# Optimization experiments

Measured on AMD Instinct MI355X. Metric: run time of the kernel, lower is better.

The kernel has to match this reference:

```python
import jax, jax.numpy as jnp
import numpy as np
from jax import lax

WHISPER_DIM, WAVLM_DIM, MUQ_DIM = 1280, 1024, 1024
CODEBOOK_SIZE, CODEBOOK_DIM = 8192, 256
B, T_W, T_M = 8, 2048, 1024  # T_w = T_wl = 2048 @50Hz, muq @25Hz -> T_m = 1024
CONCAT_DIM = WHISPER_DIM + WAVLM_DIM + MUQ_DIM


def setup_inputs() -> dict:
    key = jax.random.key(0)
    ks = jax.random.split(key, 10)
    s = 0.02
    return {
        "whisper_feat": jax.random.normal(ks[0], (B, T_W, WHISPER_DIM), jnp.float32),
        "wavlm_feat": jax.random.normal(ks[1], (B, T_W, WAVLM_DIM), jnp.float32),
        "muq_feat": jax.random.normal(ks[2], (B, T_M, MUQ_DIM), jnp.float32),
        # Conv1d weights, torch layout (out_ch, in_ch, k)
        "w_conv_w": jax.random.normal(ks[3], (WHISPER_DIM, WHISPER_DIM, 4), jnp.float32) * s,
        "w_conv_b": jnp.zeros((WHISPER_DIM,), jnp.float32),
        "wl_conv_w": jax.random.normal(ks[4], (WAVLM_DIM, WAVLM_DIM, 4), jnp.float32) * s,
        "wl_conv_b": jnp.zeros((WAVLM_DIM,), jnp.float32),
        # Linear: torch layout (out_features, in_features)
        "proj_w": jax.random.normal(ks[5], (CODEBOOK_DIM, CONCAT_DIM), jnp.float32) * s,
        "proj_b": jnp.zeros((CODEBOOK_DIM,), jnp.float32),
        "codebook": jax.random.normal(ks[6], (CODEBOOK_SIZE, CODEBOOK_DIM), jnp.float32) * 0.02,
    }


def _conv1d_s2(x_btc, w_oik, b):
    # x: (B, T, C) -> (B, C, T) conv k=4 s=2 p=1 -> (B, T//2, C)
    y = lax.conv_general_dilated(
        x_btc.transpose(0, 2, 1), w_oik,
        window_strides=(2,), padding=[(1, 1)],
        dimension_numbers=("NCH", "OIH", "NCH"))
    return (y + b[None, :, None]).transpose(0, 2, 1)


def reference(whisper_feat, wavlm_feat, muq_feat, w_conv_w, w_conv_b,
              wl_conv_w, wl_conv_b, proj_w, proj_b, codebook):
    w = _conv1d_s2(whisper_feat, w_conv_w, w_conv_b)   # (B, 1024, 1280)
    wl = _conv1d_s2(wavlm_feat, wl_conv_w, wl_conv_b)  # (B, 1024, 1024)
    m = muq_feat                                        # (B, 1024, 1024)
    min_len = min(w.shape[1], wl.shape[1], m.shape[1])
    concat = jnp.concatenate([w[:, :min_len], wl[:, :min_len], m[:, :min_len]], axis=-1)
    z_e = jnp.einsum("btc,dc->btd", concat, proj_w) + proj_b  # (B, T, D)

    # VQ: squared-Euclidean argmin against the codebook (same argmin as cdist)
    Bsz, T, D = z_e.shape
    z_flat = z_e.reshape(-1, D)
    d2 = (jnp.sum(z_flat * z_flat, axis=-1, keepdims=True)
          - 2.0 * z_flat @ codebook.T
          + jnp.sum(codebook * codebook, axis=-1)[None, :])  # (B*T, K)
    codes = jnp.argmin(d2, axis=-1)                     # (B*T,)
    z_q = codebook[codes].reshape(Bsz, T, D)
    z_q_st = z_e + lax.stop_gradient(z_q - z_e)
    commit_loss = jnp.mean(jnp.square(z_e - lax.stop_gradient(z_q)))
    return z_q_st, codes.reshape(Bsz, T), commit_loss
```

## Files before the change

kernel.cpp:

```cpp
#include <hip/hip_runtime.h>
#include <cstdint>
#include <cstddef>

typedef unsigned short u16;
typedef __attribute__((ext_vector_type(8))) short bf16x8;
typedef __attribute__((ext_vector_type(4))) float f32x4;
typedef unsigned int u32;
typedef __attribute__((address_space(1))) const u32 gu32;
typedef __attribute__((address_space(3))) u32 lu32;

__device__ __forceinline__ void gload_lds16(const void* g, void* l) {
    __builtin_amdgcn_global_load_lds((gu32*)g, (lu32*)l, 16, 0, 0);
}

__device__ __forceinline__ u16 f2bf(float v) {
    u32 u = __float_as_uint(v);
    return (u16)((u + 0x7fffu + ((u >> 16) & 1u)) >> 16);
}
__device__ __forceinline__ float bf2f(u16 h) { return __uint_as_float(((u32)h) << 16); }

__device__ __forceinline__ void split3(float f, u16& h1, u16& h2, u16& h3) {
    h1 = f2bf(f); float r = f - bf2f(h1);
    h2 = f2bf(r); r -= bf2f(h2);
    h3 = f2bf(r);
}

__device__ __forceinline__ void mfma6(f32x4& c, bf16x8 a1, bf16x8 a2, bf16x8 a3,
                                      bf16x8 b1, bf16x8 b2, bf16x8 b3) {
    c = __builtin_amdgcn_mfma_f32_16x16x32_bf16(a1, b1, c, 0, 0, 0);
    c = __builtin_amdgcn_mfma_f32_16x16x32_bf16(a1, b2, c, 0, 0, 0);
    c = __builtin_amdgcn_mfma_f32_16x16x32_bf16(a2, b1, c, 0, 0, 0);
    c = __builtin_amdgcn_mfma_f32_16x16x32_bf16(a1, b3, c, 0, 0, 0);
    c = __builtin_amdgcn_mfma_f32_16x16x32_bf16(a3, b1, c, 0, 0, 0);
    c = __builtin_amdgcn_mfma_f32_16x16x32_bf16(a2, b2, c, 0, 0, 0);
}

__global__ __launch_bounds__(256)
void split_x8t(const float* __restrict__ x, u16* __restrict__ p0,
               size_t pstr, int I) {
    __shared__ u16 tl[12288];
    const int b = blockIdx.x / 33, blk = blockIdx.x - b * 33;
    const int o0 = blk * 64;
    const int nval = (o0 + 64 <= 2050) ? 64 : (2050 - o0);
    const int c0 = blockIdx.y << 6;
    const int tid = threadIdx.x;
    const int r = tid >> 2, c4 = tid & 3;

    if (r < nval) {
        int local = o0 + r;
        int parity = local >= 1025 ? 1 : 0;
        int idx = local - parity * 1025;
        int prow = 2 * idx + parity;
        bool pad = (prow == 0) || (prow == 2049);
        int s = pad ? 0 : (prow - 1);
        const float* src = x + (size_t)(b * 2048 + s) * I + c0;
#pragma unroll
        for (int k = 0; k < 4; k++) {
            int cf4 = c4 + k * 4;
            float4 v = make_float4(0.f, 0.f, 0.f, 0.f);
            if (!pad) v = *reinterpret_cast<const float4*>(src + cf4 * 4);
            float vals[4] = {v.x, v.y, v.z, v.w};
            int base = ((cf4 >> 1) * 64 + r) * 8 + (cf4 & 1) * 4;
#pragma unroll
            for (int q = 0; q < 4; q++) {
                u16 h1, h2, h3; split3(vals[q], h1, h2, h3);
                tl[base + q]        = h1;
                tl[4096 + base + q] = h2;
                tl[8192 + base + q] = h3;
            }
        }
    }
    __syncthreads();
#pragma unroll
    for (int e = tid; e < 1536; e += 256) {
        int p = e >> 9, rem = e & 511;
        int gs = rem >> 6, rr = rem & 63;
        if (rr < nval) {
            size_t dst = (size_t)p * pstr +
                         (size_t)((c0 >> 3) + gs) * 131200 +
                         (size_t)(b * 2050 + o0 + rr) * 8;
            *reinterpret_cast<bf16x8*>(&p0[dst]) =
                *reinterpret_cast<const bf16x8*>(&tl[p * 4096 + (gs * 64 + rr) * 8]);
        }
    }
}

__global__ __launch_bounds__(256)
void split_rows8t(const float* __restrict__ in, u16* __restrict__ p0,
                  size_t pstr, int R, int C) {
    __shared__ u16 tl[12288];
    const int r0 = blockIdx.x << 6;
    const int c0 = blockIdx.y << 6;
    const int tid = threadIdx.x;
    const int r = tid >> 2, c4 = tid & 3;
    const float* src = in + (size_t)(r0 + r) * C + c0;
#pragma unroll
    for (int k = 0; k < 4; k++) {
        int cf4 = c4 + k * 4;
        float4 v = *reinterpret_cast<const float4*>(src + cf4 * 4);
        float vals[4] = {v.x, v.y, v.z, v.w};
        int base = ((cf4 >> 1) * 64 + r) * 8 + (cf4 & 1) * 4;
#pragma unroll
        for (int q = 0; q < 4; q++) {
            u16 h1, h2, h3; split3(vals[q], h1, h2, h3);
            tl[base + q]        = h1;
            tl[4096 + base + q] = h2;
            tl[8192 + base + q] = h3;
        }
    }
    __syncthreads();
#pragma unroll
    for (int e = tid; e < 1536; e += 256) {
        int p = e >> 9, rem = e & 511;
        int gs = rem >> 6, rr = rem & 63;
        size_t dst = (size_t)p * pstr +
                     ((size_t)((c0 >> 3) + gs) * R + (r0 + rr)) * 8;
        *reinterpret_cast<bf16x8*>(&p0[dst]) =
            *reinterpret_cast<const bf16x8*>(&tl[p * 4096 + (gs * 64 + rr) * 8]);
    }
}

__global__ __launch_bounds__(256)
void split_weightT8t(const float* __restrict__ w, u16* __restrict__ p0,
                     size_t pstr, int I, int O) {
    __shared__ u16 tl[12288];
    const int o0 = blockIdx.x << 6;
    const int c0 = blockIdx.y << 6;
    const int G = I >> 3;
    const int tid = threadIdx.x;
    const int r = tid >> 2, c4 = tid & 3;
    for (int kcv = 0; kcv < 4; kcv++) {
#pragma unroll
        for (int k = 0; k < 4; k++) {
            int cf4 = c4 + k * 4;
#pragma unroll
            for (int q = 0; q < 4; q++) {
                int i = c0 + cf4 * 4 + q;
                float f = w[((size_t)(o0 + r) * I + i) * 4 + kcv];
                u16 h1, h2, h3; split3(f, h1, h2, h3);
                int base = ((cf4 >> 1) * 64 + r) * 8 + (cf4 & 1) * 4 + q;
                tl[base]        = h1;
                tl[4096 + base] = h2;
                tl[8192 + base] = h3;
            }
        }
        __syncthreads();
        for (int e = tid; e < 1536; e += 256) {
            int p = e >> 9, rem = e & 511;
            int gs = rem >> 6, rr = rem & 63;
            size_t dst = (size_t)p * pstr +
                         ((size_t)(kcv * G + (c0 >> 3) + gs) * O + (o0 + rr)) * 8;
            *reinterpret_cast<bf16x8*>(&p0[dst]) =
                *reinterpret_cast<const bf16x8*>(&tl[p * 4096 + (gs * 64 + rr) * 8]);
        }
        __syncthreads();
    }
}

__global__ void cnorm_kernel(const float* __restrict__ cb, float* __restrict__ cn) {
    int w = threadIdx.x >> 6, lane = threadIdx.x & 63;
    int row = blockIdx.x * 4 + w;
    float4 v = *reinterpret_cast<const float4*>(&cb[(size_t)row * 256 + lane * 4]);
    float s = v.x * v.x + v.y * v.y + v.z * v.z + v.w * v.w;
#pragma unroll
    for (int off = 32; off; off >>= 1) s += __shfl_xor(s, off);
    if (lane == 0) cn[row] = s;
}

__global__ __launch_bounds__(256, 2)
void conv_mfma6(const u16* __restrict__ xs, unsigned pstr_x,
                const u16* __restrict__ wt, unsigned pstr_w,
                const float* __restrict__ bias,
                u16* __restrict__ outp, unsigned pstr_o,
                int I, int O) {
    __shared__ u16 lds[32768];
    const int m0 = blockIdx.x << 7;
    const int n0 = blockIdx.y << 7;
    const int tid = threadIdx.x, lane = tid & 63, wv = tid >> 6;
    const int wr = ((wv >> 1) & 1) << 6, wc = (wv & 1) << 6;
    const int fr = lane & 15, fkg = lane >> 4;
    const int b = m0 >> 10, t0 = m0 & 1023;
    const int G = I >> 3;
    const int SL = 131200;
    const int NIT = G;
    const int npt = G >> 2;

    const u16* srcp[8];
    int dsto[8];
    int inc;
#pragma unroll
    for (int j = 0; j < 8; j++) {
        int kg = j >> 1, half = j & 1;
        int r = half * 64 + lane;
        if (wv < 2) {
            srcp[j] = xs + (size_t)wv * pstr_x + (size_t)kg * SL +
                      (size_t)(b * 2050 + t0 + r) * 8;
        } else {
            srcp[j] = wt + (size_t)(wv - 2) * pstr_w + (size_t)kg * (O * 8) +
                      (size_t)(n0 + r) * 8;
        }
        dsto[j] = wv * 4096 + j * 512;
    }
    inc = (wv < 2) ? 4 * SL : O * 32;

    const u16* pa3 = xs + 2 * (size_t)pstr_x + (size_t)fkg * SL +
                     (size_t)(b * 2050 + t0 + wr + fr) * 8;
    const u16* pb3 = wt + 2 * (size_t)pstr_w + (size_t)fkg * (O * 8) +
                     (size_t)(n0 + wc + fr) * 8;

    f32x4 acc[4][4];
#pragma unroll
    for (int i = 0; i < 4; i++)
#pragma unroll
        for (int j = 0; j < 4; j++) acc[i][j] = (f32x4){0.f, 0.f, 0.f, 0.f};

#pragma unroll
    for (int j = 0; j < 8; j++) {
        gload_lds16(srcp[j], &lds[dsto[j]]);
        srcp[j] += inc;
    }
    __syncthreads();

    int scnt = npt - 1, skcv = 0;
    int dcnt = npt, dkcv = 0;
    int cur = 0;

    for (int it = 0; it < NIT; ++it) {
        const u16* lb = &lds[cur * 16384];
        bf16x8 a1[4], a2[4], b1[4], b2[4];
#pragma unroll
        for (int fm = 0; fm < 4; fm++) {
            int aidx = fkg * 1024 + (wr + fm * 16 + fr) * 8;
            a1[fm] = *reinterpret_cast<const bf16x8*>(lb + aidx);
            a2[fm] = *reinterpret_cast<const bf16x8*>(lb + 4096 + aidx);
        }
#pragma unroll
        for (int fn = 0; fn < 4; fn++) {
            int bidx = fkg * 1024 + (wc + fn * 16 + fr) * 8;
            b1[fn] = *reinterpret_cast<const bf16x8*>(lb + 8192 + bidx);
            b2[fn] = *reinterpret_cast<const bf16x8*>(lb + 12288 + bidx);
        }
        if (it + 1 < NIT) {
#pragma unroll
            for (int j = 0; j < 8; j++) {
                gload_lds16(srcp[j], &lds[(cur ^ 1) * 16384 + dsto[j]]);
                srcp[j] += inc;
            }
            if (wv < 2) {
                if (--scnt == 0) {
                    int d = ((skcv == 1) ? -8192 : 8200) - (int)pstr_x;
#pragma unroll
                    for (int j = 0; j < 8; j++) srcp[j] += d;
                    skcv++; scnt = npt;
                }
            }
        }
        bf16x8 da3[4], db3[4];
#pragma unroll
        for (int fm = 0; fm < 4; fm++)
            da3[fm] = *reinterpret_cast<const bf16x8*>(pa3 + fm * 128);
#pragma unroll
        for (int fn = 0; fn < 4; fn++)
            db3[fn] = *reinterpret_cast<const bf16x8*>(pb3 + fn * 128);
        pa3 += 4 * SL;
        pb3 += O * 32;
        if (--dcnt == 0) {
            pa3 += ((dkcv == 1) ? -8192 : 8200) - (int)pstr_x;
            dkcv++; dcnt = npt;
        }
#pragma unroll
        for (int fm = 0; fm < 4; fm++)
#pragma unroll
            for (int fn = 0; fn < 4; fn++)
                mfma6(acc[fm][fn], a1[fm], a2[fm], da3[fm],
                      b1[fn], b2[fn], db3[fn]);
        __syncthreads();
        cur ^= 1;
    }

    u16 (*eld)[32][132] = (u16 (*)[32][132])lds;
    float bv[4];
#pragma unroll
    for (int fn = 0; fn < 4; fn++) bv[fn] = bias[n0 + wc + fn * 16 + fr];
    const int srb = (wr >> 6) * 16 + fkg * 4;
#pragma unroll
    for (int fm = 0; fm < 4; fm++) {
#pragma unroll
        for (int fn = 0; fn < 4; fn++) {
            int cl = wc + fn * 16 + fr;
#pragma unroll
            for (int j = 0; j < 4; j++) {
                float f = acc[fm][fn][j] + bv[fn];
                u16 h1, h2, h3; split3(f, h1, h2, h3);
                eld[0][srb + j][cl] = h1;
                eld[1][srb + j][cl] = h2;
                eld[2][srb + j][cl] = h3;
            }
        }
        __syncthreads();
#pragma unroll
        for (int q = 0; q < 6; q++) {
            int e = q * 256 + tid;
            int g = e / 96, rem = e - g * 96;
            int p = rem >> 5, sr = rem & 31;
            bf16x8 vv = *reinterpret_cast<const bf16x8*>(&eld[p][sr][g * 8]);
            int rowg = m0 + ((sr >> 4) << 6) + fm * 16 + (sr & 15);
            size_t addr = (size_t)p * pstr_o +
                          (size_t)((n0 >> 3) + g) * 65536 + (size_t)rowg * 8;
            *reinterpret_cast<bf16x8*>(&outp[addr]) = vv;
        }
        __syncthreads();
    }
}

__global__ __launch_bounds__(256, 3)
void proj_mfma5(const u16* __restrict__ sA, const u16* __restrict__ sB,
                const u16* __restrict__ sM, const u16* __restrict__ wp,
                const float* __restrict__ bias, float* __restrict__ z_e,
                u16* __restrict__ zpl) {
    __shared__ u16 lds[24576];
    const int m0 = blockIdx.x << 7;
    const int n0 = blockIdx.y << 7;
    const int tid = threadIdx.x, lane = tid & 63, wv = tid >> 6;
    const int wr = ((wv >> 1) & 1) << 6, wc = (wv & 1) << 6;
    const int fr = lane & 15, fkg = lane >> 4;

    const u16* srcp[12];
    int dsto[12];
#pragma unroll
    for (int j = 0; j < 12; j++) {
        int ii = wv * 12 + j;
        int tile = ii >> 3, sub = ii & 7;
        int kg = sub >> 1, half = sub & 1;
        int r = half * 64 + lane;
        if (tile >= 3)
            srcp[j] = wp + (size_t)(tile - 3) * 851968 + (size_t)kg * 2048 +
                      (size_t)(n0 + r) * 8;
        else
            srcp[j] = nullptr;
        dsto[j] = tile * 4096 + sub * 512;
    }

    f32x4 acc[4][4];
#pragma unroll
    for (int i = 0; i < 4; i++)
#pragma unroll
        for (int j = 0; j < 4; j++) acc[i][j] = (f32x4){0.f, 0.f, 0.f, 0.f};

    const u16* segp[3] = {sA, sB, sM};
    const int segG[3] = {160, 128, 128};
    const unsigned segP[3] = {10485760u, 8388608u, 8388608u};

    for (int seg = 0; seg < 3; seg++) {
        const u16* sp = segp[seg];
        const unsigned sps = segP[seg];
#pragma unroll
        for (int j = 0; j < 12; j++) {
            int ii = wv * 12 + j;
            int tile = ii >> 3, sub = ii & 7;
            int kg = sub >> 1, half = sub & 1;
            int r = half * 64 + lane;
            if (tile < 3)
                srcp[j] = sp + (size_t)tile * sps + (size_t)kg * 65536 +
                          (size_t)(m0 + r) * 8;
        }
        const int niter = segG[seg] >> 2;
        for (int it = 0; it < niter; it++) {
#pragma unroll
            for (int j = 0; j < 12; j++) {
                gload_lds16(srcp[j], &lds[dsto[j]]);
                int ii = wv * 12 + j;
                srcp[j] += (ii >> 3) < 3 ? 262144 : 8192;
            }
            __syncthreads();
            bf16x8 bfr[3][4];
#pragma unroll
            for (int p = 0; p < 3; p++)
#pragma unroll
                for (int fn = 0; fn < 4; fn++)
                    bfr[p][fn] = *reinterpret_cast<const bf16x8*>(
                        &lds[(3 + p) * 4096 + fkg * 1024 + (wc + fn * 16 + fr) * 8]);
#pragma unroll
            for (int fm = 0; fm < 4; fm++) {
                int aidx = fkg * 1024 + (wr + fm * 16 + fr) * 8;
                bf16x8 a1 = *reinterpret_cast<const bf16x8*>(&lds[aidx]);
                bf16x8 a2 = *reinterpret_cast<const bf16x8*>(&lds[4096 + aidx]);
                bf16x8 a3 = *reinterpret_cast<const bf16x8*>(&lds[8192 + aidx]);
#pragma unroll
                for (int fn = 0; fn < 4; fn++)
                    mfma6(acc[fm][fn], a1, a2, a3, bfr[0][fn], bfr[1][fn], bfr[2][fn]);
            }
            __syncthreads();
        }
    }
    u16 (*eld)[32][132] = (u16 (*)[32][132])lds;
    float bv[4];
#pragma unroll
    for (int fn = 0; fn < 4; fn++) bv[fn] = bias[n0 + wc + fn * 16 + fr];
    const int srb = (wr >> 6) * 16 + fkg * 4;
#pragma unroll
    for (int fm = 0; fm < 4; fm++) {
#pragma unroll
        for (int fn = 0; fn < 4; fn++) {
            int cl = wc + fn * 16 + fr;
            int col = n0 + cl;
#pragma unroll
            for (int j = 0; j < 4; j++) {
                float f = acc[fm][fn][j] + bv[fn];
                int rowg = m0 + wr + fm * 16 + fkg * 4 + j;
                z_e[(size_t)rowg * 256 + col] = f;
                u16 h1, h2, h3; split3(f, h1, h2, h3);
                eld[0][srb + j][cl] = h1;
                eld[1][srb + j][cl] = h2;
                eld[2][srb + j][cl] = h3;
            }
        }
        __syncthreads();
#pragma unroll
        for (int q = 0; q < 6; q++) {
            int e = q * 256 + tid;
            int g = e / 96, rem = e - g * 96;
            int p = rem >> 5, sr = rem & 31;
            bf16x8 vv = *reinterpret_cast<const bf16x8*>(&eld[p][sr][g * 8]);
            int rowg = m0 + ((sr >> 4) << 6) + fm * 16 + (sr & 15);
            size_t addr = (size_t)p * 2097152 +
                          (size_t)((n0 >> 3) + g) * 65536 + (size_t)rowg * 8;
            *reinterpret_cast<bf16x8*>(&zpl[addr]) = vv;
        }
        __syncthreads();
    }
}

__global__ __launch_bounds__(256, 3)
void vq_mfma4(const u16* __restrict__ zpl, const u16* __restrict__ cbpl,
              const float* __restrict__ cn, double* __restrict__ pmin,
              int* __restrict__ pidx) {
    __shared__ __align__(16) char smem[49152];
    u16* lds = (u16*)smem;
    const int m0 = blockIdx.x << 7;
    const int n0 = blockIdx.y << 7;
    const int tid = threadIdx.x, lane = tid & 63, wv = tid >> 6;
    const int wr = ((wv >> 1) & 1) << 6, wc = (wv & 1) << 6;
    const int fr = lane & 15, fkg = lane >> 4;

    const u16* srcp[12];
    int dsto[12];
#pragma unroll
    for (int j = 0; j < 12; j++) {
        int ii = wv * 12 + j;
        int tile = ii >> 3, sub = ii & 7;
        int kg = sub >> 1, half = sub & 1;
        int r = half * 64 + lane;
        if (tile < 3)
            srcp[j] = zpl + (size_t)tile * 2097152 + (size_t)kg * 65536 +
                      (size_t)(m0 + r) * 8;
        else
            srcp[j] = cbpl + (size_t)(tile - 3) * 2097152 + (size_t)kg * 65536 +
                      (size_t)(n0 + r) * 8;
        dsto[j] = tile * 4096 + sub * 512;
    }

    f32x4 acc[4][4];
#pragma unroll
    for (int i = 0; i < 4; i++)
#pragma unroll
        for (int j = 0; j < 4; j++) acc[i][j] = (f32x4){0.f, 0.f, 0.f, 0.f};

    for (int kt = 0; kt < 256; kt += 32) {
#pragma unroll
        for (int j = 0; j < 12; j++) {
            gload_lds16(srcp[j], &lds[dsto[j]]);
            srcp[j] += 262144;
        }
        __syncthreads();
        bf16x8 bfr[3][4];
#pragma unroll
        for (int p = 0; p < 3; p++)
#pragma unroll
            for (int fn = 0; fn < 4; fn++)
                bfr[p][fn] = *reinterpret_cast<const bf16x8*>(
                    &lds[(3 + p) * 4096 + fkg * 1024 + (wc + fn * 16 + fr) * 8]);
#pragma unroll
        for (int fm = 0; fm < 4; fm++) {
            int aidx = fkg * 1024 + (wr + fm * 16 + fr) * 8;
            bf16x8 a1 = *reinterpret_cast<const bf16x8*>(&lds[aidx]);
            bf16x8 a2 = *reinterpret_cast<const bf16x8*>(&lds[4096 + aidx]);
            bf16x8 a3 = *reinterpret_cast<const bf16x8*>(&lds[8192 + aidx]);
#pragma unroll
            for (int fn = 0; fn < 4; fn++)
                mfma6(acc[fm][fn], a1, a2, a3, bfr[0][fn], bfr[1][fn], bfr[2][fn]);
        }
        __syncthreads();
    }
    double (*red_d)[32] = (double (*)[32])smem;
    int (*red_n)[32] = (int (*)[32])(smem + 32768);
#pragma unroll
    for (int fm = 0; fm < 4; fm++)
#pragma unroll
        for (int j = 0; j < 4; j++) {
            double best = 1e300; int bestn = 0x7fffffff;
#pragma unroll
            for (int fn = 0; fn < 4; fn++) {
                int gn = n0 + wc + fn * 16 + fr;
                double d = (double)cn[gn] - 2.0 * (double)acc[fm][fn][j];
                if (d < best || (d == best && gn < bestn)) { best = d; bestn = gn; }
            }
            int row = wr + fm * 16 + fkg * 4 + j;
            int cand = ((wv & 1) << 4) + fr;
            red_d[row][cand] = best; red_n[row][cand] = bestn;
        }
    __syncthreads();
    if (tid < 128) {
        double best = red_d[tid][0]; int bestn = red_n[tid][0];
#pragma unroll 4
        for (int k = 1; k < 32; k++) {
            double d = red_d[tid][k]; int n2 = red_n[tid][k];
            if (d < best || (d == best && n2 < bestn)) { best = d; bestn = n2; }
        }
        size_t idx = (size_t)(m0 + tid) * 64 + (n0 >> 7);
        pmin[idx] = best; pidx[idx] = bestn;
    }
}

__global__ void vq_finalize(const double* __restrict__ pmin, const int* __restrict__ pidx,
                            const float* __restrict__ z, const float* __restrict__ cb,
                            float* __restrict__ out, double* __restrict__ cpart) {
    int w = threadIdx.x >> 6, lane = threadIdx.x & 63;
    int m = blockIdx.x * 4 + w;
    double d = pmin[(size_t)m * 64 + lane];
    int n = pidx[(size_t)m * 64 + lane];
#pragma unroll
    for (int off = 32; off; off >>= 1) {
        double d2 = __shfl_xor(d, off);
        int n2 = __shfl_xor(n, off);
        if (d2 < d || (d2 == d && n2 < n)) { d = d2; n = n2; }
    }
    float4 cv = *reinterpret_cast<const float4*>(&cb[(size_t)n * 256 + lane * 4]);
    float4 zv = *reinterpret_cast<const float4*>(&z[(size_t)m * 256 + lane * 4]);
    *reinterpret_cast<float4*>(&out[(size_t)m * 256 + lane * 4]) = cv;
    float dx = zv.x - cv.x, dy = zv.y - cv.y, dz = zv.z - cv.z, dw = zv.w - cv.w;
    double s = (double)(dx * dx) + (double)(dy * dy) + (double)(dz * dz) + (double)(dw * dw);
#pragma unroll
    for (int off = 32; off; off >>= 1) s += __shfl_xor(s, off);
    if (lane == 0) {
        out[2097152 + m] = (float)n;
        cpart[m] = s;
    }
}

__global__ void vq_reduce(const double* __restrict__ cpart, float* __restrict__ out) {
    __shared__ double sm[256];
    double s = 0.0;
    for (int i = threadIdx.x; i < 8192; i += 256) s += cpart[i];
    sm[threadIdx.x] = s;
    __syncthreads();
    for (int off = 128; off; off >>= 1) {
        if ((int)threadIdx.x < off) sm[threadIdx.x] += sm[threadIdx.x + off];
        __syncthreads();
    }
    if (threadIdx.x == 0) out[2105344] = (float)(sm[0] / 2097152.0);
}

extern "C" void kernel_launch(void* const* d_in, const int* in_sizes, int n_in,
                              void* d_out, int out_size, void* d_ws, size_t ws_size,
                              hipStream_t stream) {
    (void)in_sizes; (void)n_in; (void)out_size; (void)ws_size;
    const float* whisper   = (const float*)d_in[0];
    const float* wavlm     = (const float*)d_in[1];
    const float* muq       = (const float*)d_in[2];
    const float* w_conv_w  = (const float*)d_in[3];
    const float* w_conv_b  = (const float*)d_in[4];
    const float* wl_conv_w = (const float*)d_in[5];
    const float* wl_conv_b = (const float*)d_in[6];
    const float* proj_w    = (const float*)d_in[7];
    const float* proj_b    = (const float*)d_in[8];
    const float* codebook  = (const float*)d_in[9];
    float* out = (float*)d_out;
    char* wsb = (char*)d_ws;

    u16*   xsA   = (u16*)(wsb + 0);
    u16*   wtbA  = (u16*)(wsb + 125952000);
    u16*   cApl  = (u16*)(wsb + 176259072);
    u16*   xsB   = (u16*)(wsb + 0);
    u16*   wtbB  = (u16*)(wsb + 100761600);
    u16*   cBpl  = (u16*)(wsb + 125927424);
    u16*   muqpl = (u16*)(wsb + 0);
    u16*   wtpPl = (u16*)(wsb + 50331648);
    float* z_e   = (float*)(wsb + 55443456);
    u16*   zpl   = (u16*)(wsb + 63832064);
    u16*   cbpl  = (u16*)(wsb + 76414976);
    float* cnorm = (float*)(wsb + 88997888);
    double* pmin = (double*)(wsb + 89030656);
    int*    pidx = (int*)(wsb + 93224960);
    double* cpart= (double*)(wsb + 95322112);

    split_x8t<<<dim3(264, 20), 256, 0, stream>>>(whisper, xsA, 20992000, 1280);
    split_weightT8t<<<dim3(20, 20), 256, 0, stream>>>(w_conv_w, wtbA, 6553600, 1280, 1280);
    conv_mfma6<<<dim3(64, 10), 256, 0, stream>>>(xsA, 20992000, wtbA, 6553600,
                                                 w_conv_b, cApl, 10485760, 1280, 1280);
    split_x8t<<<dim3(264, 16), 256, 0, stream>>>(wavlm, xsB, 16793600, 1024);
    split_weightT8t<<<dim3(16, 16), 256, 0, stream>>>(wl_conv_w, wtbB, 4194304, 1024, 1024);
    conv_mfma6<<<dim3(64, 8), 256, 0, stream>>>(xsB, 16793600, wtbB, 4194304,
                                                wl_conv_b, cBpl, 8388608, 1024, 1024);
    split_rows8t<<<dim3(128, 16), 256, 0, stream>>>(muq, muqpl, 8388608, 8192, 1024);
    split_rows8t<<<dim3(4, 52), 256, 0, stream>>>(proj_w, wtpPl, 851968, 256, 3328);
    proj_mfma5<<<dim3(64, 2), 256, 0, stream>>>(cApl, cBpl, muqpl, wtpPl, proj_b, z_e, zpl);
    split_rows8t<<<dim3(128, 4), 256, 0, stream>>>(codebook, cbpl, 2097152, 8192, 256);
    cnorm_kernel<<<2048, 256, 0, stream>>>(codebook, cnorm);
    vq_mfma4<<<dim3(64, 64), 256, 0, stream>>>(zpl, cbpl, cnorm, pmin, pidx);
    vq_finalize<<<2048, 256, 0, stream>>>(pmin, pidx, z_e, codebook, out, cpart);
    vq_reduce<<<1, 256, 0, stream>>>(cpart, out);
}
```

Baseline: 1.372 ms.

## Template conv GEMM on N-tile width and pack weights into contiguous per-tile slabs

The conv GEMM kernel now takes its N-tile width as a template parameter. The whisper conv uses 160-wide tiles, so its grid is 64x8 = 512 blocks instead of 64x10 = 640, matching the wavlm conv's block count. The weight-split kernel now writes weights into per-N-tile slabs, so each tile's B data for one k-group is contiguous and loads linearly into LDS. This aims to reduce block-count tail effects and improve load coalescing. The cost is a larger LDS footprint and more accumulators per wave for the 160 case, which could lower occupancy.

```diff
diff --git a/kernel.cpp b/kernel.cpp
--- a/kernel.cpp
+++ b/kernel.cpp
@@ -121,12 +121,13 @@
 }
 
 __global__ __launch_bounds__(256)
-void split_weightT8t(const float* __restrict__ w, u16* __restrict__ p0,
-                     size_t pstr, int I, int O) {
+void split_weightT8m(const float* __restrict__ w, u16* __restrict__ p0,
+                     size_t pstr, int I, int O, int NT) {
     __shared__ u16 tl[12288];
     const int o0 = blockIdx.x << 6;
     const int c0 = blockIdx.y << 6;
     const int G = I >> 3;
+    const size_t SLAB = (size_t)4 * G * NT * 8;
     const int tid = threadIdx.x;
     const int r = tid >> 2, c4 = tid & 3;
     for (int kcv = 0; kcv < 4; kcv++) {
@@ -148,8 +149,11 @@
         for (int e = tid; e < 1536; e += 256) {
             int p = e >> 9, rem = e & 511;
             int gs = rem >> 6, rr = rem & 63;
-            size_t dst = (size_t)p * pstr +
-                         ((size_t)(kcv * G + (c0 >> 3) + gs) * O + (o0 + rr)) * 8;
+            int o = o0 + rr;
+            int ng = o / NT, orr = o - ng * NT;
+            int kg = kcv * G + (c0 >> 3) + gs;
+            size_t dst = (size_t)p * pstr + (size_t)ng * SLAB +
+                         (size_t)kg * NT * 8 + (size_t)orr * 8;
             *reinterpret_cast<bf16x8*>(&p0[dst]) =
                 *reinterpret_cast<const bf16x8*>(&tl[p * 4096 + (gs * 64 + rr) * 8]);
         }
@@ -167,58 +171,70 @@
     if (lane == 0) cn[row] = s;
 }
 
+template<int TN>
 __global__ __launch_bounds__(256, 2)
-void conv_mfma6(const u16* __restrict__ xs, unsigned pstr_x,
+void conv_mfma7(const u16* __restrict__ xs, unsigned pstr_x,
                 const u16* __restrict__ wt, unsigned pstr_w,
                 const float* __restrict__ bias,
                 u16* __restrict__ outp, unsigned pstr_o,
                 int I, int O) {
-    __shared__ u16 lds[32768];
+    constexpr int FN = TN / 32;
+    constexpr int NB = TN / 16;
+    constexpr int BPLANE = 32 * TN;
+    constexpr int BUFE = 8192 + 2 * BPLANE;
+    __shared__ u16 lds[2 * BUFE];
     const int m0 = blockIdx.x << 7;
-    const int n0 = blockIdx.y << 7;
+    const int ny = blockIdx.y;
+    const int n0 = ny * TN;
     const int tid = threadIdx.x, lane = tid & 63, wv = tid >> 6;
-    const int wr = ((wv >> 1) & 1) << 6, wc = (wv & 1) << 6;
+    const int wr = ((wv >> 1) & 1) << 6, wc = (wv & 1) * (TN / 2);
     const int fr = lane & 15, fkg = lane >> 4;
     const int b = m0 >> 10, t0 = m0 & 1023;
     const int G = I >> 3;
     const int SL = 131200;
-    const int NIT = G;
-    const int npt = G >> 2;
-
-    const u16* srcp[8];
-    int dsto[8];
+    const int NIT = G, npt = G >> 2;
+    const size_t SLAB = (size_t)4 * G * TN * 8;
+
+    const u16* srcp[NB];
+    int dsto[NB];
+    const int nload = (wv < 2) ? 8 : NB;
     int inc;
-#pragma unroll
-    for (int j = 0; j < 8; j++) {
-        int kg = j >> 1, half = j & 1;
-        int r = half * 64 + lane;
-        if (wv < 2) {
-            srcp[j] = xs + (size_t)wv * pstr_x + (size_t)kg * SL +
-                      (size_t)(b * 2050 + t0 + r) * 8;
-        } else {
-            srcp[j] = wt + (size_t)(wv - 2) * pstr_w + (size_t)kg * (O * 8) +
-                      (size_t)(n0 + r) * 8;
-        }
-        dsto[j] = wv * 4096 + j * 512;
-    }
-    inc = (wv < 2) ? 4 * SL : O * 32;
+    if (wv < 2) {
+        inc = 4 * SL;
+#pragma unroll
+        for (int j = 0; j < NB; j++) {
+            if (j < 8) {
+                int kg = j >> 1, half = j & 1;
+                int r = half * 64 + lane;
+                srcp[j] = xs + (size_t)wv * pstr_x + (size_t)kg * SL +
+                          (size_t)(b * 2050 + t0 + r) * 8;
+                dsto[j] = wv * 4096 + j * 512;
+            } else { srcp[j] = xs; dsto[j] = 0; }
+        }
+    } else {
+        inc = BPLANE;
+#pragma unroll
+        for (int j = 0; j < NB; j++) {
+            srcp[j] = wt + (size_t)(wv - 2) * pstr_w + (size_t)ny * SLAB +
+                      j * 512 + lane * 8;
+            dsto[j] = 8192 + (wv - 2) * BPLANE + j * 512;
+        }
+    }
 
     const u16* pa3 = xs + 2 * (size_t)pstr_x + (size_t)fkg * SL +
                      (size_t)(b * 2050 + t0 + wr + fr) * 8;
-    const u16* pb3 = wt + 2 * (size_t)pstr_w + (size_t)fkg * (O * 8) +
-                     (size_t)(n0 + wc + fr) * 8;
-
-    f32x4 acc[4][4];
+    const u16* pb3 = wt + 2 * (size_t)pstr_w + (size_t)ny * SLAB +
+                     (size_t)fkg * (TN * 8) + (size_t)(wc + fr) * 8;
+
+    f32x4 acc[4][FN];
 #pragma unroll
     for (int i = 0; i < 4; i++)
 #pragma unroll
-        for (int j = 0; j < 4; j++) acc[i][j] = (f32x4){0.f, 0.f, 0.f, 0.f};
-
-#pragma unroll
-    for (int j = 0; j < 8; j++) {
-        gload_lds16(srcp[j], &lds[dsto[j]]);
-        srcp[j] += inc;
-    }
+        for (int j = 0; j < FN; j++) acc[i][j] = (f32x4){0.f, 0.f, 0.f, 0.f};
+
+#pragma unroll
+    for (int j = 0; j < NB; j++)
+        if (j < nload) { gload_lds16(srcp[j], &lds[dsto[j]]); srcp[j] += inc; }
     __syncthreads();
 
     int scnt = npt - 1, skcv = 0;
@@ -226,8 +242,8 @@
     int cur = 0;
 
     for (int it = 0; it < NIT; ++it) {
-        const u16* lb = &lds[cur * 16384];
-        bf16x8 a1[4], a2[4], b1[4], b2[4];
+        const u16* lb = &lds[cur * BUFE];
+        bf16x8 a1[4], a2[4], b1[FN], b2[FN];
 #pragma unroll
         for (int fm = 0; fm < 4; fm++) {
             int aidx = fkg * 1024 + (wr + fm * 16 + fr) * 8;
@@ -235,17 +251,18 @@
             a2[fm] = *reinterpret_cast<const bf16x8*>(lb + 4096 + aidx);
         }
 #pragma unroll
-        for (int fn = 0; fn < 4; fn++) {
-            int bidx = fkg * 1024 + (wc + fn * 16 + fr) * 8;
-            b1[fn] = *reinterpret_cast<const bf16x8*>(lb + 8192 + bidx);
-            b2[fn] = *reinterpret_cast<const bf16x8*>(lb + 12288 + bidx);
+        for (int fn = 0; fn < FN; fn++) {
+            int bidx = 8192 + fkg * (TN * 8) + (wc + fn * 16 + fr) * 8;
+            b1[fn] = *reinterpret_cast<const bf16x8*>(lb + bidx);
+            b2[fn] = *reinterpret_cast<const bf16x8*>(lb + BPLANE + bidx);
         }
         if (it + 1 < NIT) {
 #pragma unroll
-            for (int j = 0; j < 8; j++) {
-                gload_lds16(srcp[j], &lds[(cur ^ 1) * 16384 + dsto[j]]);
-                srcp[j] += inc;
-            }
+            for (int j = 0; j < NB; j++)
+                if (j < nload) {
+                    gload_lds16(srcp[j], &lds[(cur ^ 1) * BUFE + dsto[j]]);
+                    srcp[j] += inc;
+                }
             if (wv < 2) {
                 if (--scnt == 0) {
                     int d = ((skcv == 1) ? -8192 : 8200) - (int)pstr_x;
@@ -255,15 +272,15 @@
                 }
             }
         }
-        bf16x8 da3[4], db3[4];
+        bf16x8 da3[4], db3[FN];
 #pragma unroll
         for (int fm = 0; fm < 4; fm++)
             da3[fm] = *reinterpret_cast<const bf16x8*>(pa3 + fm * 128);
 #pragma unroll
-        for (int fn = 0; fn < 4; fn++)
+        for (int fn = 0; fn < FN; fn++)
             db3[fn] = *reinterpret_cast<const bf16x8*>(pb3 + fn * 128);
         pa3 += 4 * SL;
-        pb3 += O * 32;
+        pb3 += BPLANE;
         if (--dcnt == 0) {
             pa3 += ((dkcv == 1) ? -8192 : 8200) - (int)pstr_x;
             dkcv++; dcnt = npt;
@@ -271,22 +288,22 @@
 #pragma unroll
         for (int fm = 0; fm < 4; fm++)
 #pragma unroll
-            for (int fn = 0; fn < 4; fn++)
+            for (int fn = 0; fn < FN; fn++)
                 mfma6(acc[fm][fn], a1[fm], a2[fm], da3[fm],
                       b1[fn], b2[fn], db3[fn]);
         __syncthreads();
         cur ^= 1;
     }
 
-    u16 (*eld)[32][132] = (u16 (*)[32][132])lds;
-    float bv[4];
-#pragma unroll
-    for (int fn = 0; fn < 4; fn++) bv[fn] = bias[n0 + wc + fn * 16 + fr];
+    u16 (*eld)[32][TN + 8] = (u16 (*)[32][TN + 8])lds;
+    float bv[FN];
+#pragma unroll
+    for (int fn = 0; fn < FN; fn++) bv[fn] = bias[n0 + wc + fn * 16 + fr];
     const int srb = (wr >> 6) * 16 + fkg * 4;
 #pragma unroll
     for (int fm = 0; fm < 4; fm++) {
 #pragma unroll
-        for (int fn = 0; fn < 4; fn++) {
+        for (int fn = 0; fn < FN; fn++) {
             int cl = wc + fn * 16 + fr;
 #pragma unroll
             for (int j = 0; j < 4; j++) {
@@ -298,9 +315,7 @@
             }
         }
         __syncthreads();
-#pragma unroll
-        for (int q = 0; q < 6; q++) {
-            int e = q * 256 + tid;
+        for (int e = tid; e < 96 * (TN / 8); e += 256) {
             int g = e / 96, rem = e - g * 96;
             int p = rem >> 5, sr = rem & 31;
             bf16x8 vv = *reinterpret_cast<const bf16x8*>(&eld[p][sr][g * 8]);
@@ -595,13 +610,17 @@
     double* cpart= (double*)(wsb + 95322112);
 
     split_x8t<<<dim3(264, 20), 256, 0, stream>>>(whisper, xsA, 20992000, 1280);
-    split_weightT8t<<<dim3(20, 20), 256, 0, stream>>>(w_conv_w, wtbA, 6553600, 1280, 1280);
-    conv_mfma6<<<dim3(64, 10), 256, 0, stream>>>(xsA, 20992000, wtbA, 6553600,
-                                                 w_conv_b, cApl, 10485760, 1280, 1280);
+    split_weightT8m<<<dim3(20, 20), 256, 0, stream>>>(w_conv_w, wtbA, 6553600,
+                                                      1280, 1280, 160);
+    conv_mfma7<160><<<dim3(64, 8), 256, 0, stream>>>(xsA, 20992000, wtbA, 6553600,
+                                                     w_conv_b, cApl, 10485760,
+                                                     1280, 1280);
     split_x8t<<<dim3(264, 16), 256, 0, stream>>>(wavlm, xsB, 16793600, 1024);
-    split_weightT8t<<<dim3(16, 16), 256, 0, stream>>>(wl_conv_w, wtbB, 4194304, 1024, 1024);
-    conv_mfma6<<<dim3(64, 8), 256, 0, stream>>>(xsB, 16793600, wtbB, 4194304,
-                                                wl_conv_b, cBpl, 8388608, 1024, 1024);
+    split_weightT8m<<<dim3(16, 16), 256, 0, stream>>>(wl_conv_w, wtbB, 4194304,
+                                                      1024, 1024, 128);
+    conv_mfma7<128><<<dim3(64, 8), 256, 0, stream>>>(xsB, 16793600, wtbB, 4194304,
+                                                     wl_conv_b, cBpl, 8388608,
+                                                     1024, 1024);
     split_rows8t<<<dim3(128, 16), 256, 0, stream>>>(muq, muqpl, 8388608, 8192, 1024);
     split_rows8t<<<dim3(4, 52), 256, 0, stream>>>(proj_w, wtpPl, 851968, 256, 3328);
     proj_mfma5<<<dim3(64, 2), 256, 0, stream>>>(cApl, cBpl, muqpl, wtpPl, proj_b, z_e, zpl);
```

New measurement: 1.269 ms. 7.5% less time.
